# Optimization experiments

Measured on AMD Instinct MI355X. Metric: run time of the kernel, lower is better.

The kernel has to match this reference:

```python
import jax, jax.numpy as jnp
import numpy as np

NEG_SLOPE = 0.25


def _gcn_layer(x, W, b, edge_row, edge_col, edge_weight, n_nodes):
    # support = x @ W  (dense GEMM)
    support = x @ W  # [N, out]
    # sparse.mm(adj, support): out[i] = sum_{(i,j) in E} w_ij * support[j]
    msgs = edge_weight[:, None] * support[edge_col]          # [E, out] gather
    out = jax.ops.segment_sum(msgs, edge_row, num_segments=n_nodes)  # scatter-add
    return out + b


def setup_inputs() -> dict:
    key = jax.random.key(0)
    ks = jax.random.split(key, 8)
    N, E = 100000, 1000000
    d_in, d1, d2, d3 = 64, 64, 32, 16
    x = jax.random.normal(ks[0], (N, d_in), dtype=jnp.float32)
    edge_row = jax.random.randint(ks[1], (E,), 0, N, dtype=jnp.int32)
    edge_col = jax.random.randint(ks[2], (E,), 0, N, dtype=jnp.int32)
    edge_weight = jax.random.uniform(ks[3], (E,), dtype=jnp.float32)
    # Xavier-normal-ish init for weights, zero bias (matches module init)
    W1 = jax.random.normal(ks[4], (d_in, d1), dtype=jnp.float32) * np.sqrt(2.0 / (d_in + d1))
    W2 = jax.random.normal(ks[5], (d1, d2), dtype=jnp.float32) * np.sqrt(2.0 / (d1 + d2))
    W3 = jax.random.normal(ks[6], (d2, d3), dtype=jnp.float32) * np.sqrt(2.0 / (d2 + d3))
    b1 = jnp.zeros((d1,), jnp.float32)
    b2 = jnp.zeros((d2,), jnp.float32)
    b3 = jnp.zeros((d3,), jnp.float32)
    return {"x": x, "edge_row": edge_row, "edge_col": edge_col,
            "edge_weight": edge_weight, "W1": W1, "b1": b1,
            "W2": W2, "b2": b2, "W3": W3, "b3": b3}


def reference(x, edge_row, edge_col, edge_weight, W1, b1, W2, b2, W3, b3):
    n_nodes = x.shape[0]
    h = _gcn_layer(x, W1, b1, edge_row, edge_col, edge_weight, n_nodes)
    h = jax.nn.leaky_relu(h, NEG_SLOPE)
    # dropout: eval mode -> identity
    h = _gcn_layer(h, W2, b2, edge_row, edge_col, edge_weight, n_nodes)
    h = jax.nn.leaky_relu(h, NEG_SLOPE)
    h = _gcn_layer(h, W3, b3, edge_row, edge_col, edge_weight, n_nodes)
    h = jax.nn.leaky_relu(h, NEG_SLOPE)
    return h
```

## Files before the change

kernel.cpp:

```cpp
#include <hip/hip_runtime.h>
#include <hip/hip_bf16.h>


typedef short bf16x8 __attribute__((ext_vector_type(8)));
typedef float f32x4 __attribute__((ext_vector_type(4)));

__device__ __forceinline__ float lrelu(float v) { return v > 0.0f ? v : 0.25f * v; }
__device__ __forceinline__ float bflo(unsigned u) { return __uint_as_float(u << 16); }
__device__ __forceinline__ float bfhi(unsigned u) { return __uint_as_float(u & 0xffff0000u); }
__device__ __forceinline__ unsigned short f2bf(float f) {
    unsigned u = __float_as_uint(f);
    return (unsigned short)((u + 0x7fffu + ((u >> 16) & 1u)) >> 16);
}
__device__ __forceinline__ unsigned packbf(float a, float b) {
    return (unsigned)f2bf(a) | ((unsigned)f2bf(b) << 16);
}


constexpr int SCAN_T = 256;
constexpr int SCAN_PER = 8;
constexpr int SCAN_CHUNK = SCAN_T * SCAN_PER;
constexpr int CHUNK = 4096;
constexpr int BKT_BITS = 7;
constexpr int BKTSZ = 128;
constexpr int MAXBKT = 1024;
constexpr int MAXNSC = 128;

__device__ __forceinline__ void build_bofs(const int* __restrict__ bsum, int nsc,
                                           int* tmp, int* bofs) {
    int t = threadIdx.x;
    int v = (t < MAXNSC && t < nsc) ? bsum[t] : 0;
    if (t < MAXNSC) tmp[t] = v;
    __syncthreads();
    for (int off = 1; off < MAXNSC; off <<= 1) {
        int add = (t < MAXNSC && t >= off) ? tmp[t - off] : 0;
        __syncthreads();
        if (t < MAXNSC) tmp[t] += add;
        __syncthreads();
    }
    if (t < MAXNSC) bofs[t] = tmp[t] - v;
    __syncthreads();
}

__device__ __forceinline__ int getI(const int* __restrict__ I,
                                    const int* __restrict__ bofs, size_t idx) {
    return I[idx] + bofs[idx >> 11];
}

__global__ void __launch_bounds__(256)
hist1_kernel(const int* __restrict__ row, int* __restrict__ hists,
             int E, int nbkt, int NB) {
    __shared__ int hist[MAXBKT];
    for (int i = threadIdx.x; i < nbkt; i += 256) hist[i] = 0;
    __syncthreads();
    int e0 = blockIdx.x * CHUNK;
    int e1 = min(e0 + CHUNK, E);
    for (int e = e0 + threadIdx.x; e < e1; e += 256)
        atomicAdd(&hist[row[e] >> BKT_BITS], 1);
    __syncthreads();
    for (int i = threadIdx.x; i < nbkt; i += 256)
        hists[(size_t)i * NB + blockIdx.x] = hist[i];
}

__global__ void __launch_bounds__(SCAN_T)
scan1_kernel(int* __restrict__ I, int* __restrict__ bsum, int T) {
    __shared__ int lds[SCAN_T];
    int t = threadIdx.x;
    int base = blockIdx.x * SCAN_CHUNK + t * SCAN_PER;
    int v[SCAN_PER];
    int run = 0;
#pragma unroll
    for (int j = 0; j < SCAN_PER; ++j) {
        int i = base + j;
        run += (i < T) ? I[i] : 0;
        v[j] = run;
    }
    lds[t] = run;
    __syncthreads();
    for (int off = 1; off < SCAN_T; off <<= 1) {
        int add = (t >= off) ? lds[t - off] : 0;
        __syncthreads();
        lds[t] += add;
        __syncthreads();
    }
    int excl = lds[t] - run;
#pragma unroll
    for (int j = 0; j < SCAN_PER; ++j) {
        int i = base + j;
        if (i < T) I[i] = v[j] + excl;
    }
    if (t == SCAN_T - 1) bsum[blockIdx.x] = lds[t];
}

__global__ void __launch_bounds__(256)
place1_kernel(const int* __restrict__ row, const int* __restrict__ col,
              const float* __restrict__ w, const int* __restrict__ I,
              const int* __restrict__ bsum, int nsc, int2* __restrict__ eb1,
              int E, int nbkt, int NB) {
    __shared__ int srow[CHUNK];
    __shared__ int hist[MAXBKT];
    __shared__ int tmp[MAXNSC];
    __shared__ int bofs[MAXNSC];
    build_bofs(bsum, nsc, tmp, bofs);
    for (int i = threadIdx.x; i < nbkt; i += 256) hist[i] = 0;
    int e0 = blockIdx.x * CHUNK;
    int e1 = min(e0 + CHUNK, E);
    for (int e = e0 + threadIdx.x; e < e1; e += 256) srow[e - e0] = row[e];
    __syncthreads();
    for (int i = threadIdx.x; i < e1 - e0; i += 256)
        atomicAdd(&hist[srow[i] >> BKT_BITS], 1);
    __syncthreads();
    for (int i = threadIdx.x; i < nbkt; i += 256) {
        size_t idx = (size_t)i * NB + blockIdx.x;
        hist[i] = getI(I, bofs, idx) - hist[i];
    }
    __syncthreads();
    for (int e = e0 + threadIdx.x; e < e1; e += 256) {
        int r = srow[e - e0];
        int pos = atomicAdd(&hist[r >> BKT_BITS], 1);
        eb1[pos] = make_int2(((r & (BKTSZ - 1)) << 20) | col[e], __float_as_int(w[e]));
    }
}

__global__ void __launch_bounds__(256)
place2_kernel(const int2* __restrict__ eb1, const int* __restrict__ I,
              const int* __restrict__ bsum, int nsc, unsigned* __restrict__ edges,
              int* __restrict__ rs, int N, int NB) {
    __shared__ int hist[BKTSZ];
    __shared__ int scanv[BKTSZ];
    __shared__ int tmp[MAXNSC];
    __shared__ int bofs[MAXNSC];
    build_bofs(bsum, nsc, tmp, bofs);
    int b = blockIdx.x;
    int t = threadIdx.x;
    int bstart = (b == 0) ? 0 : getI(I, bofs, (size_t)b * NB - 1);
    int bend   = getI(I, bofs, (size_t)(b + 1) * NB - 1);
    if (t < BKTSZ) hist[t] = 0;
    __syncthreads();
    for (int e = bstart + t; e < bend; e += 256)
        atomicAdd(&hist[(eb1[e].x >> 20) & (BKTSZ - 1)], 1);
    __syncthreads();
    int cval = (t < BKTSZ) ? hist[t] : 0;
    if (t < BKTSZ) scanv[t] = cval;
    __syncthreads();
    for (int off = 1; off < BKTSZ; off <<= 1) {
        int add = (t < BKTSZ && t >= off) ? scanv[t - off] : 0;
        __syncthreads();
        if (t < BKTSZ) scanv[t] += add;
        __syncthreads();
    }
    if (t < BKTSZ) {
        int gnode = b * BKTSZ + t;
        if (gnode < N) rs[gnode] = bstart + scanv[t];
        hist[t] = bstart + scanv[t] - cval;
    }
    __syncthreads();
    for (int e = bstart + t; e < bend; e += 256) {
        int2 ev = eb1[e];
        int lrow = (ev.x >> 20) & (BKTSZ - 1);
        float w = __int_as_float(ev.y);
        unsigned q = (unsigned)(w * 32768.f + 0.5f);
        q = q > 32767u ? 32767u : q;
        unsigned packed = (q << 17) | (unsigned)(ev.x & 0x1FFFF);
        int pos = atomicAdd(&hist[lrow], 1);
        edges[pos] = packed;
    }
}


template <int K, int M, int NT, bool INF32>
__global__ void __launch_bounds__(256)
mfma_gemm_kernel(const void* __restrict__ inv, const float* __restrict__ W,
                 __hip_bfloat16* __restrict__ out, int N) {
    constexpr int CT = M / 16;
    constexpr int KH = K / 32;
    __shared__ float Ws[K * M];
    for (int i = threadIdx.x; i < K * M / 4; i += 256)
        reinterpret_cast<float4*>(Ws)[i] = reinterpret_cast<const float4*>(W)[i];
    __syncthreads();

    const int lane = threadIdx.x & 63;
    const int wave = threadIdx.x >> 6;
    const int lrow = lane & 15;
    const int lgrp = lane >> 4;

    bf16x8 bfrag[CT][KH];
#pragma unroll
    for (int ct = 0; ct < CT; ++ct)
#pragma unroll
        for (int kh = 0; kh < KH; ++kh)
#pragma unroll
            for (int j = 0; j < 8; ++j)
                bfrag[ct][kh][j] =
                    (short)f2bf(Ws[(kh * 32 + lgrp * 8 + j) * M + ct * 16 + lrow]);

    const float* inf = (const float*)inv;
    const unsigned short* inb = (const unsigned short*)inv;
    unsigned short* outs = (unsigned short*)out;

    const int wave_base = blockIdx.x * (4 * NT * 16) + wave * (NT * 16);
#pragma unroll
    for (int t = 0; t < NT; ++t) {
        int nb = wave_base + t * 16;
        if (nb >= N) break;
        int arow = nb + lrow;

        bf16x8 afrag[KH];
#pragma unroll
        for (int kh = 0; kh < KH; ++kh) {
            if constexpr (INF32) {
                const float* ap = inf + (size_t)arow * K + kh * 32 + lgrp * 8;
                float4 u0 = *reinterpret_cast<const float4*>(ap);
                float4 u1 = *reinterpret_cast<const float4*>(ap + 4);
                afrag[kh][0] = (short)f2bf(u0.x); afrag[kh][1] = (short)f2bf(u0.y);
                afrag[kh][2] = (short)f2bf(u0.z); afrag[kh][3] = (short)f2bf(u0.w);
                afrag[kh][4] = (short)f2bf(u1.x); afrag[kh][5] = (short)f2bf(u1.y);
                afrag[kh][6] = (short)f2bf(u1.z); afrag[kh][7] = (short)f2bf(u1.w);
            } else {
                afrag[kh] = *reinterpret_cast<const bf16x8*>(
                    inb + (size_t)arow * K + kh * 32 + lgrp * 8);
            }
        }

        f32x4 acc[CT];
#pragma unroll
        for (int ct = 0; ct < CT; ++ct) { acc[ct][0]=0.f; acc[ct][1]=0.f; acc[ct][2]=0.f; acc[ct][3]=0.f; }
#pragma unroll
        for (int ct = 0; ct < CT; ++ct)
#pragma unroll
            for (int kh = 0; kh < KH; ++kh)
                acc[ct] = __builtin_amdgcn_mfma_f32_16x16x32_bf16(
                    afrag[kh], bfrag[ct][kh], acc[ct], 0, 0, 0);

#pragma unroll
        for (int ct = 0; ct < CT; ++ct)
#pragma unroll
            for (int r = 0; r < 4; ++r) {
                int orow = nb + lgrp * 4 + r;
                outs[(size_t)orow * M + ct * 16 + lrow] = f2bf(acc[ct][r]);
            }
    }
}


template <int M, int G, bool ACTOUT, bool OUTBF16>
__global__ void __launch_bounds__(256)
agg_kernel(const int* __restrict__ rs, const unsigned* __restrict__ edges,
           const __hip_bfloat16* __restrict__ sup, const float* __restrict__ b,
           void* __restrict__ outv, int N) {
    constexpr int VPT = M / G;
    constexpr int EB = 8;
    constexpr int NE = EB / G;
    static_assert(VPT == 8 || VPT == 4, "VPT must be 8 or 4");
    int tid = blockIdx.x * blockDim.x + threadIdx.x;
    int node = tid / G;
    if (node >= N) return;
    int g = tid - node * G;

    float acc[VPT];
#pragma unroll
    for (int j = 0; j < VPT; ++j) acc[j] = b[g * VPT + j];

    int beg = node ? rs[node - 1] : 0;
    int end = rs[node];
    const unsigned short* su = reinterpret_cast<const unsigned short*>(sup) + g * VPT;

    using gvec = typename std::conditional<VPT == 8, uint4, uint2>::type;

    for (int j0 = beg; j0 < end; j0 += EB) {
        unsigned p[NE];
#pragma unroll
        for (int k = 0; k < NE; ++k) {
            int jl = j0 + k * G + g;
            p[k] = edges[jl < end ? jl : end - 1];
        }
        int cnt = min(EB, end - j0);
        gvec gv[EB];
        float wv[EB];
#pragma unroll
        for (int jj = 0; jj < EB; ++jj) {
            unsigned pe = __shfl(p[jj / G], jj % G, G);
            wv[jj] = (float)(pe >> 17) * (1.0f / 32768.f);
            unsigned col = pe & 0x1FFFFu;
            if (jj < cnt)
                gv[jj] = *reinterpret_cast<const gvec*>(su + (size_t)col * M);
        }
#pragma unroll
        for (int jj = 0; jj < EB; ++jj) {
            if (jj >= cnt) break;
            float w = wv[jj];
            if constexpr (VPT == 8) {
                acc[0] += w * bflo(gv[jj].x); acc[1] += w * bfhi(gv[jj].x);
                acc[2] += w * bflo(gv[jj].y); acc[3] += w * bfhi(gv[jj].y);
                acc[4] += w * bflo(gv[jj].z); acc[5] += w * bfhi(gv[jj].z);
                acc[6] += w * bflo(gv[jj].w); acc[7] += w * bfhi(gv[jj].w);
            } else {
                acc[0] += w * bflo(gv[jj].x); acc[1] += w * bfhi(gv[jj].x);
                acc[2] += w * bflo(gv[jj].y); acc[3] += w * bfhi(gv[jj].y);
            }
        }
    }
    if (ACTOUT) {
#pragma unroll
        for (int j = 0; j < VPT; ++j) acc[j] = lrelu(acc[j]);
    }
    if constexpr (OUTBF16) {
        __hip_bfloat16* out = (__hip_bfloat16*)outv;
        if constexpr (VPT == 8) {
            uint4 o = { packbf(acc[0], acc[1]), packbf(acc[2], acc[3]),
                        packbf(acc[4], acc[5]), packbf(acc[6], acc[7]) };
            *reinterpret_cast<uint4*>(out + (size_t)node * M + g * 8) = o;
        } else {
            uint2 o = { packbf(acc[0], acc[1]), packbf(acc[2], acc[3]) };
            *reinterpret_cast<uint2*>(out + (size_t)node * M + g * 4) = o;
        }
    } else {
        float* out = (float*)outv;
        if constexpr (VPT == 8) {
            float4 o0 = {acc[0], acc[1], acc[2], acc[3]};
            float4 o1 = {acc[4], acc[5], acc[6], acc[7]};
            reinterpret_cast<float4*>(out + (size_t)node * M + g * 8)[0] = o0;
            reinterpret_cast<float4*>(out + (size_t)node * M + g * 8)[1] = o1;
        } else {
            float4 o = {acc[0], acc[1], acc[2], acc[3]};
            *reinterpret_cast<float4*>(out + (size_t)node * M + g * 4) = o;
        }
    }
}

extern "C" void kernel_launch(void* const* d_in, const int* in_sizes, int n_in,
                              void* d_out, int out_size, void* d_ws, size_t ws_size,
                              hipStream_t stream) {
    const float* x    = (const float*)d_in[0];
    const int*   erow = (const int*)  d_in[1];
    const int*   ecol = (const int*)  d_in[2];
    const float* ew   = (const float*)d_in[3];
    const float* W1   = (const float*)d_in[4];
    const float* b1   = (const float*)d_in[5];
    const float* W2   = (const float*)d_in[6];
    const float* b2   = (const float*)d_in[7];
    const float* W3   = (const float*)d_in[8];
    const float* b3   = (const float*)d_in[9];
    float* out = (float*)d_out;

    const int N = in_sizes[0] / 64;
    const int E = in_sizes[1];

    auto cdiv = [](long a, long b) { return (int)((a + b - 1) / b); };
    const int NB   = cdiv(E, CHUNK);
    const int nbkt = cdiv(N, BKTSZ);
    const long T   = (long)nbkt * NB;
    const int nsc  = cdiv(T, SCAN_CHUNK);

    char* wsc = (char*)d_ws;
    const size_t SZ64B = (size_t)N * 64 * 2;
    const size_t SZ32B = (size_t)N * 32 * 2;
    __hip_bfloat16* s1 = (__hip_bfloat16*)(wsc);
    __hip_bfloat16* a1 = (__hip_bfloat16*)(wsc + SZ64B);
    __hip_bfloat16* s2 = (__hip_bfloat16*)(wsc + 2 * SZ64B);
    __hip_bfloat16* a2 = (__hip_bfloat16*)(wsc + SZ64B);
    __hip_bfloat16* s3 = (__hip_bfloat16*)(wsc);

    char* csr = wsc + 2 * SZ64B + SZ32B;
    int*      I     = (int*)csr;
    int*      bsum  = I + T;
    int*      rs    = bsum + MAXNSC;
    int2*     eb1   = (int2*)(rs + N);
    unsigned* edges = (unsigned*)(eb1 + E);

    const int B = 256;
    constexpr int NT = 2;
    const int GB = cdiv(N, 4 * NT * 16);

    hist1_kernel<<<NB, B, 0, stream>>>(erow, I, E, nbkt, NB);
    scan1_kernel<<<nsc, SCAN_T, 0, stream>>>(I, bsum, (int)T);
    place1_kernel<<<NB, B, 0, stream>>>(erow, ecol, ew, I, bsum, nsc, eb1, E, nbkt, NB);
    place2_kernel<<<nbkt, B, 0, stream>>>(eb1, I, bsum, nsc, edges, rs, N, NB);

    mfma_gemm_kernel<64, 64, NT, true><<<GB, B, 0, stream>>>(x, W1, s1, N);
    agg_kernel<64, 8, true, true><<<cdiv((long)N * 8, B), B, 0, stream>>>(rs, edges, s1, b1, a1, N);

    mfma_gemm_kernel<64, 32, NT, false><<<GB, B, 0, stream>>>(a1, W2, s2, N);
    agg_kernel<32, 4, true, true><<<cdiv((long)N * 4, B), B, 0, stream>>>(rs, edges, s2, b2, a2, N);

    mfma_gemm_kernel<32, 16, NT, false><<<GB, B, 0, stream>>>(a2, W3, s3, N);
    agg_kernel<16, 4, true, false><<<cdiv((long)N * 4, B), B, 0, stream>>>(rs, edges, s3, b3, out, N);
}
```

Measured before the change: 106.9 us.

## Fuse aggregation with next-layer GEMM and merge histogram with first GEMM

Each sparse aggregation kernel now writes its activated result into shared memory and immediately multiplies it by the next layer's weight with MFMA, so the intermediate activations are never written to or read back from global memory. The edge histogram pass and the first dense GEMM are merged into one launch by splitting the grid between the two roles. This removes two launches and intermediate memory traffic, at the cost of extra LDS per block and a short GEMM phase after the gather in each fused kernel.

Measured after the change: 95.93 us. -10.3%, faster.

```diff
diff --git a/kernel.cpp b/kernel.cpp
--- a/kernel.cpp
+++ b/kernel.cpp
@@ -45,21 +45,6 @@
 __device__ __forceinline__ int getI(const int* __restrict__ I,
                                     const int* __restrict__ bofs, size_t idx) {
     return I[idx] + bofs[idx >> 11];
-}
-
-__global__ void __launch_bounds__(256)
-hist1_kernel(const int* __restrict__ row, int* __restrict__ hists,
-             int E, int nbkt, int NB) {
-    __shared__ int hist[MAXBKT];
-    for (int i = threadIdx.x; i < nbkt; i += 256) hist[i] = 0;
-    __syncthreads();
-    int e0 = blockIdx.x * CHUNK;
-    int e1 = min(e0 + CHUNK, E);
-    for (int e = e0 + threadIdx.x; e < e1; e += 256)
-        atomicAdd(&hist[row[e] >> BKT_BITS], 1);
-    __syncthreads();
-    for (int i = threadIdx.x; i < nbkt; i += 256)
-        hists[(size_t)i * NB + blockIdx.x] = hist[i];
 }
 
 __global__ void __launch_bounds__(SCAN_T)
@@ -168,17 +153,29 @@
 }
 
 
-template <int K, int M, int NT, bool INF32>
 __global__ void __launch_bounds__(256)
-mfma_gemm_kernel(const void* __restrict__ inv, const float* __restrict__ W,
-                 __hip_bfloat16* __restrict__ out, int N) {
-    constexpr int CT = M / 16;
-    constexpr int KH = K / 32;
-    __shared__ float Ws[K * M];
+fused_hist_gemm1_kernel(const int* __restrict__ row, int* __restrict__ hists,
+                        int E, int nbkt, int NB,
+                        const float* __restrict__ x, const float* __restrict__ W1,
+                        __hip_bfloat16* __restrict__ s1, int N) {
+    __shared__ float Ws[64 * 64];
+    if ((int)blockIdx.x < NB) {
+        int* hist = reinterpret_cast<int*>(Ws);
+        for (int i = threadIdx.x; i < nbkt; i += 256) hist[i] = 0;
+        __syncthreads();
+        int e0 = blockIdx.x * CHUNK;
+        int e1 = min(e0 + CHUNK, E);
+        for (int e = e0 + threadIdx.x; e < e1; e += 256)
+            atomicAdd(&hist[row[e] >> BKT_BITS], 1);
+        __syncthreads();
+        for (int i = threadIdx.x; i < nbkt; i += 256)
+            hists[(size_t)i * NB + blockIdx.x] = hist[i];
+        return;
+    }
+    constexpr int K = 64, M = 64, NT = 2, CT = M / 16, KH = K / 32;
     for (int i = threadIdx.x; i < K * M / 4; i += 256)
-        reinterpret_cast<float4*>(Ws)[i] = reinterpret_cast<const float4*>(W)[i];
-    __syncthreads();
-
+        reinterpret_cast<float4*>(Ws)[i] = reinterpret_cast<const float4*>(W1)[i];
+    __syncthreads();
     const int lane = threadIdx.x & 63;
     const int wave = threadIdx.x >> 6;
     const int lrow = lane & 15;
@@ -194,34 +191,24 @@
                 bfrag[ct][kh][j] =
                     (short)f2bf(Ws[(kh * 32 + lgrp * 8 + j) * M + ct * 16 + lrow]);
 
-    const float* inf = (const float*)inv;
-    const unsigned short* inb = (const unsigned short*)inv;
-    unsigned short* outs = (unsigned short*)out;
-
-    const int wave_base = blockIdx.x * (4 * NT * 16) + wave * (NT * 16);
+    unsigned short* outs = (unsigned short*)s1;
+    const int wave_base = ((int)blockIdx.x - NB) * (4 * NT * 16) + wave * (NT * 16);
 #pragma unroll
     for (int t = 0; t < NT; ++t) {
         int nb = wave_base + t * 16;
         if (nb >= N) break;
         int arow = nb + lrow;
-
         bf16x8 afrag[KH];
 #pragma unroll
         for (int kh = 0; kh < KH; ++kh) {
-            if constexpr (INF32) {
-                const float* ap = inf + (size_t)arow * K + kh * 32 + lgrp * 8;
-                float4 u0 = *reinterpret_cast<const float4*>(ap);
-                float4 u1 = *reinterpret_cast<const float4*>(ap + 4);
-                afrag[kh][0] = (short)f2bf(u0.x); afrag[kh][1] = (short)f2bf(u0.y);
-                afrag[kh][2] = (short)f2bf(u0.z); afrag[kh][3] = (short)f2bf(u0.w);
-                afrag[kh][4] = (short)f2bf(u1.x); afrag[kh][5] = (short)f2bf(u1.y);
-                afrag[kh][6] = (short)f2bf(u1.z); afrag[kh][7] = (short)f2bf(u1.w);
-            } else {
-                afrag[kh] = *reinterpret_cast<const bf16x8*>(
-                    inb + (size_t)arow * K + kh * 32 + lgrp * 8);
-            }
+            const float* ap = x + (size_t)arow * K + kh * 32 + lgrp * 8;
+            float4 u0 = *reinterpret_cast<const float4*>(ap);
+            float4 u1 = *reinterpret_cast<const float4*>(ap + 4);
+            afrag[kh][0] = (short)f2bf(u0.x); afrag[kh][1] = (short)f2bf(u0.y);
+            afrag[kh][2] = (short)f2bf(u0.z); afrag[kh][3] = (short)f2bf(u0.w);
+            afrag[kh][4] = (short)f2bf(u1.x); afrag[kh][5] = (short)f2bf(u1.y);
+            afrag[kh][6] = (short)f2bf(u1.z); afrag[kh][7] = (short)f2bf(u1.w);
         }
-
         f32x4 acc[CT];
 #pragma unroll
         for (int ct = 0; ct < CT; ++ct) { acc[ct][0]=0.f; acc[ct][1]=0.f; acc[ct][2]=0.f; acc[ct][3]=0.f; }
@@ -231,7 +218,6 @@
             for (int kh = 0; kh < KH; ++kh)
                 acc[ct] = __builtin_amdgcn_mfma_f32_16x16x32_bf16(
                     afrag[kh], bfrag[ct][kh], acc[ct], 0, 0, 0);
-
 #pragma unroll
         for (int ct = 0; ct < CT; ++ct)
 #pragma unroll
@@ -243,15 +229,117 @@
 }
 
 
-template <int M, int G, bool ACTOUT, bool OUTBF16>
+template <int MA, int GA, int MB>
+__global__ void __launch_bounds__(256)
+fused_agg_gemm_kernel(const int* __restrict__ rs, const unsigned* __restrict__ edges,
+                      const __hip_bfloat16* __restrict__ sup, const float* __restrict__ bias,
+                      const float* __restrict__ W, __hip_bfloat16* __restrict__ outS, int N) {
+    constexpr int VPT = MA / GA;
+    static_assert(VPT == 8, "agg phase assumes 8 bf16 per lane");
+    constexpr int NPB = 256 / GA;
+    constexpr int KH = MA / 32, CTB = MB / 16, TILES = NPB / 16;
+    static_assert(TILES * CTB == 4, "4 waves must cover (tile,ct) space");
+    constexpr int STR = MA + 8;
+    constexpr int EB = 8, NE = EB / GA;
+
+    __shared__ float WsF[MA * MB];
+    __shared__ unsigned short atile[NPB][STR];
+
+    for (int i = threadIdx.x; i < MA * MB / 4; i += 256)
+        reinterpret_cast<float4*>(WsF)[i] = reinterpret_cast<const float4*>(W)[i];
+
+    int tid = threadIdx.x;
+    int lr = tid / GA;
+    int g = tid & (GA - 1);
+    int node = blockIdx.x * NPB + lr;
+
+    float acc[VPT];
+#pragma unroll
+    for (int j = 0; j < VPT; ++j) acc[j] = bias[g * VPT + j];
+
+    if (node < N) {
+        int beg = node ? rs[node - 1] : 0;
+        int end = rs[node];
+        const unsigned short* su = reinterpret_cast<const unsigned short*>(sup) + g * VPT;
+        for (int j0 = beg; j0 < end; j0 += EB) {
+            unsigned p[NE];
+#pragma unroll
+            for (int k = 0; k < NE; ++k) {
+                int jl = j0 + k * GA + g;
+                p[k] = edges[jl < end ? jl : end - 1];
+            }
+            int cnt = min(EB, end - j0);
+            uint4 gv[EB];
+            float wv[EB];
+#pragma unroll
+            for (int jj = 0; jj < EB; ++jj) {
+                unsigned pe = __shfl(p[jj / GA], jj % GA, GA);
+                wv[jj] = (float)(pe >> 17) * (1.0f / 32768.f);
+                unsigned col = pe & 0x1FFFFu;
+                if (jj < cnt)
+                    gv[jj] = *reinterpret_cast<const uint4*>(su + (size_t)col * MA);
+            }
+#pragma unroll
+            for (int jj = 0; jj < EB; ++jj) {
+                if (jj >= cnt) break;
+                float w = wv[jj];
+                acc[0] += w * bflo(gv[jj].x); acc[1] += w * bfhi(gv[jj].x);
+                acc[2] += w * bflo(gv[jj].y); acc[3] += w * bfhi(gv[jj].y);
+                acc[4] += w * bflo(gv[jj].z); acc[5] += w * bfhi(gv[jj].z);
+                acc[6] += w * bflo(gv[jj].w); acc[7] += w * bfhi(gv[jj].w);
+            }
+        }
+    }
+#pragma unroll
+    for (int j = 0; j < VPT; ++j) acc[j] = lrelu(acc[j]);
+    uint4 pk = { packbf(acc[0], acc[1]), packbf(acc[2], acc[3]),
+                 packbf(acc[4], acc[5]), packbf(acc[6], acc[7]) };
+    *reinterpret_cast<uint4*>(&atile[lr][g * 8]) = pk;
+    __syncthreads();
+
+    const int lane = tid & 63;
+    const int wave = tid >> 6;
+    const int tile = wave / CTB;
+    const int ct = wave % CTB;
+    const int lrow = lane & 15;
+    const int lgrp = lane >> 4;
+
+    bf16x8 bfrag[KH];
+#pragma unroll
+    for (int kh = 0; kh < KH; ++kh)
+#pragma unroll
+        for (int j = 0; j < 8; ++j)
+            bfrag[kh][j] = (short)f2bf(WsF[(kh * 32 + lgrp * 8 + j) * MB + ct * 16 + lrow]);
+
+    int nb = blockIdx.x * NPB + tile * 16;
+    if (nb >= N) return;
+    bf16x8 afrag[KH];
+#pragma unroll
+    for (int kh = 0; kh < KH; ++kh)
+        afrag[kh] = *reinterpret_cast<const bf16x8*>(&atile[tile * 16 + lrow][kh * 32 + lgrp * 8]);
+
+    f32x4 a = {0.f, 0.f, 0.f, 0.f};
+#pragma unroll
+    for (int kh = 0; kh < KH; ++kh)
+        a = __builtin_amdgcn_mfma_f32_16x16x32_bf16(afrag[kh], bfrag[kh], a, 0, 0, 0);
+
+    unsigned short* outs = (unsigned short*)outS;
+#pragma unroll
+    for (int r = 0; r < 4; ++r) {
+        int orow = nb + lgrp * 4 + r;
+        outs[(size_t)orow * MB + ct * 16 + lrow] = f2bf(a[r]);
+    }
+}
+
+
+template <int M, int G, bool ACTOUT>
 __global__ void __launch_bounds__(256)
 agg_kernel(const int* __restrict__ rs, const unsigned* __restrict__ edges,
            const __hip_bfloat16* __restrict__ sup, const float* __restrict__ b,
-           void* __restrict__ outv, int N) {
+           float* __restrict__ out, int N) {
     constexpr int VPT = M / G;
     constexpr int EB = 8;
     constexpr int NE = EB / G;
-    static_assert(VPT == 8 || VPT == 4, "VPT must be 8 or 4");
     int tid = blockIdx.x * blockDim.x + threadIdx.x;
     int node = tid / G;
     if (node >= N) return;
@@ -264,8 +352,6 @@
     int beg = node ? rs[node - 1] : 0;
     int end = rs[node];
     const unsigned short* su = reinterpret_cast<const unsigned short*>(sup) + g * VPT;
-
-    using gvec = typename std::conditional<VPT == 8, uint4, uint2>::type;
 
     for (int j0 = beg; j0 < end; j0 += EB) {
         unsigned p[NE];
@@ -275,7 +361,7 @@
             p[k] = edges[jl < end ? jl : end - 1];
         }
         int cnt = min(EB, end - j0);
-        gvec gv[EB];
+        uint2 gv[EB];
         float wv[EB];
 #pragma unroll
         for (int jj = 0; jj < EB; ++jj) {
@@ -283,49 +369,22 @@
             wv[jj] = (float)(pe >> 17) * (1.0f / 32768.f);
             unsigned col = pe & 0x1FFFFu;
             if (jj < cnt)
-                gv[jj] = *reinterpret_cast<const gvec*>(su + (size_t)col * M);
+                gv[jj] = *reinterpret_cast<const uint2*>(su + (size_t)col * M);
         }
 #pragma unroll
         for (int jj = 0; jj < EB; ++jj) {
             if (jj >= cnt) break;
             float w = wv[jj];
-            if constexpr (VPT == 8) {
-                acc[0] += w * bflo(gv[jj].x); acc[1] += w * bfhi(gv[jj].x);
-                acc[2] += w * bflo(gv[jj].y); acc[3] += w * bfhi(gv[jj].y);
-                acc[4] += w * bflo(gv[jj].z); acc[5] += w * bfhi(gv[jj].z);
-                acc[6] += w * bflo(gv[jj].w); acc[7] += w * bfhi(gv[jj].w);
-            } else {
-                acc[0] += w * bflo(gv[jj].x); acc[1] += w * bfhi(gv[jj].x);
-                acc[2] += w * bflo(gv[jj].y); acc[3] += w * bfhi(gv[jj].y);
-            }
+            acc[0] += w * bflo(gv[jj].x); acc[1] += w * bfhi(gv[jj].x);
+            acc[2] += w * bflo(gv[jj].y); acc[3] += w * bfhi(gv[jj].y);
         }
     }
     if (ACTOUT) {
 #pragma unroll
         for (int j = 0; j < VPT; ++j) acc[j] = lrelu(acc[j]);
     }
-    if constexpr (OUTBF16) {
-        __hip_bfloat16* out = (__hip_bfloat16*)outv;
-        if constexpr (VPT == 8) {
-            uint4 o = { packbf(acc[0], acc[1]), packbf(acc[2], acc[3]),
-                        packbf(acc[4], acc[5]), packbf(acc[6], acc[7]) };
-            *reinterpret_cast<uint4*>(out + (size_t)node * M + g * 8) = o;
-        } else {
-            uint2 o = { packbf(acc[0], acc[1]), packbf(acc[2], acc[3]) };
-            *reinterpret_cast<uint2*>(out + (size_t)node * M + g * 4) = o;
-        }
-    } else {
-        float* out = (float*)outv;
-        if constexpr (VPT == 8) {
-            float4 o0 = {acc[0], acc[1], acc[2], acc[3]};
-            float4 o1 = {acc[4], acc[5], acc[6], acc[7]};
-            reinterpret_cast<float4*>(out + (size_t)node * M + g * 8)[0] = o0;
-            reinterpret_cast<float4*>(out + (size_t)node * M + g * 8)[1] = o1;
-        } else {
-            float4 o = {acc[0], acc[1], acc[2], acc[3]};
-            *reinterpret_cast<float4*>(out + (size_t)node * M + g * 4) = o;
-        }
-    }
+    float4 o = {acc[0], acc[1], acc[2], acc[3]};
+    *reinterpret_cast<float4*>(out + (size_t)node * M + g * 4) = o;
 }
 
 extern "C" void kernel_launch(void* const* d_in, const int* in_sizes, int n_in,
@@ -355,13 +414,12 @@
     char* wsc = (char*)d_ws;
     const size_t SZ64B = (size_t)N * 64 * 2;
     const size_t SZ32B = (size_t)N * 32 * 2;
+    const size_t SZ16B = (size_t)N * 16 * 2;
     __hip_bfloat16* s1 = (__hip_bfloat16*)(wsc);
-    __hip_bfloat16* a1 = (__hip_bfloat16*)(wsc + SZ64B);
-    __hip_bfloat16* s2 = (__hip_bfloat16*)(wsc + 2 * SZ64B);
-    __hip_bfloat16* a2 = (__hip_bfloat16*)(wsc + SZ64B);
-    __hip_bfloat16* s3 = (__hip_bfloat16*)(wsc);
-
-    char* csr = wsc + 2 * SZ64B + SZ32B;
+    __hip_bfloat16* s2 = (__hip_bfloat16*)(wsc + SZ64B);
+    __hip_bfloat16* s3 = (__hip_bfloat16*)(wsc + SZ64B + SZ32B);
+
+    char* csr = wsc + SZ64B + SZ32B + SZ16B;
     int*      I     = (int*)csr;
     int*      bsum  = I + T;
     int*      rs    = bsum + MAXNSC;
@@ -369,20 +427,18 @@
     unsigned* edges = (unsigned*)(eb1 + E);
 
     const int B = 256;
-    constexpr int NT = 2;
-    const int GB = cdiv(N, 4 * NT * 16);
-
-    hist1_kernel<<<NB, B, 0, stream>>>(erow, I, E, nbkt, NB);
+    const int GB = cdiv(N, 128);
+
+    fused_hist_gemm1_kernel<<<NB + GB, B, 0, stream>>>(erow, I, E, nbkt, NB, x, W1, s1, N);
     scan1_kernel<<<nsc, SCAN_T, 0, stream>>>(I, bsum, (int)T);
     place1_kernel<<<NB, B, 0, stream>>>(erow, ecol, ew, I, bsum, nsc, eb1, E, nbkt, NB);
     place2_kernel<<<nbkt, B, 0, stream>>>(eb1, I, bsum, nsc, edges, rs, N, NB);
 
-    mfma_gemm_kernel<64, 64, NT, true><<<GB, B, 0, stream>>>(x, W1, s1, N);
-    agg_kernel<64, 8, true, true><<<cdiv((long)N * 8, B), B, 0, stream>>>(rs, edges, s1, b1, a1, N);
-
-    mfma_gemm_kernel<64, 32, NT, false><<<GB, B, 0, stream>>>(a1, W2, s2, N);
-    agg_kernel<32, 4, true, true><<<cdiv((long)N * 4, B), B, 0, stream>>>(rs, edges, s2, b2, a2, N);
-
-    mfma_gemm_kernel<32, 16, NT, false><<<GB, B, 0, stream>>>(a2, W3, s3, N);
-    agg_kernel<16, 4, true, false><<<cdiv((long)N * 4, B), B, 0, stream>>>(rs, edges, s3, b3, out, N);
-}
+    fused_agg_gemm_kernel<64, 8, 32><<<cdiv(N, 32), B, 0, stream>>>(
+        rs, edges, s1, b1, W2, s2, N);
+
+    fused_agg_gemm_kernel<32, 4, 16><<<cdiv(N, 64), B, 0, stream>>>(
+        rs, edges, s2, b2, W3, s3, N);
+
+    agg_kernel<16, 4, true><<<cdiv((long)N * 4, B), B, 0, stream>>>(rs, edges, s3, b3, out, N);
+}
```
